# Performance work log

Hardware: AMD Instinct MI355X
Metric: run time of the kernel (lower is better)

The kernel has to match this reference:

```python
import jax, jax.numpy as jnp
import numpy as np

B, C_IN, C_OUT, T, HID = 8, 32, 32, 8192, 64


def setup_inputs() -> dict:
    key = jax.random.key(0)
    ks = jax.random.split(key, 8)
    s1 = 1.0  # fan_in=1
    s2 = 1.0 / np.sqrt(HID)
    return {
        "x": jax.random.normal(ks[0], (B, C_IN, T), dtype=jnp.float32),
        "w1": jax.random.uniform(ks[1], (1, HID), jnp.float32, -s1, s1),
        "b1": jax.random.uniform(ks[2], (HID,), jnp.float32, -s1, s1),
        "w2": jax.random.uniform(ks[3], (HID, HID), jnp.float32, -s2, s2),
        "b2": jax.random.uniform(ks[4], (HID,), jnp.float32, -s2, s2),
        "w3": jax.random.uniform(ks[5], (HID, C_IN * C_OUT), jnp.float32, -s2, s2),
        "b3": jax.random.uniform(ks[6], (C_IN * C_OUT,), jnp.float32, -s2, s2),
        "bias": jnp.zeros((C_OUT,), dtype=jnp.float32),
    }


def _filters(w1, b1, w2, b2, w3, b3):
    # positions: (T, 1) in [0, 1]
    pos = jnp.linspace(0.0, 1.0, T, dtype=jnp.float32)[:, None]
    h = jax.nn.gelu(pos @ w1 + b1, approximate=False)
    h = jax.nn.gelu(h @ w2 + b2, approximate=False)
    f = h @ w3 + b3                      # (T, out*in)
    f = f.reshape(T, C_OUT, C_IN)
    return jnp.transpose(f, (1, 2, 0))   # (out, in, T)


def reference(x, w1, b1, w2, b2, w3, b3, bias):
    freq_x = jnp.fft.rfft(x, axis=-1)                      # (B, in, F)
    filt = _filters(w1, b1, w2, b2, w3, b3)                # (out, in, T)
    freq_f = jnp.fft.rfft(filt, axis=-1)                   # (out, in, F)
    conv_freq = jnp.einsum('bif,oif->bof', freq_x, freq_f) # contract over in
    out = jnp.fft.irfft(conv_freq, n=T, axis=-1)           # (B, out, T)
    return out + bias[None, :, None]
```

## Files before the change

kernel.cpp:

```cpp
#include <hip/hip_runtime.h>
#include <math.h>

#define T 8192
#define M 4096
#define JS 4104
#define B 8
#define CIN 32
#define COUT 32
#define HID 64
#define FT 4

__device__ inline float2 cadd(float2 a, float2 b){ return make_float2(a.x+b.x, a.y+b.y); }
__device__ inline float2 csub(float2 a, float2 b){ return make_float2(a.x-b.x, a.y-b.y); }
__device__ inline float2 cmul(float2 a, float2 b){ return make_float2(a.x*b.x - a.y*b.y, a.x*b.y + a.y*b.x); }
__device__ inline float2 cmulc(float2 a, float2 b){
    return make_float2(a.x*b.x + a.y*b.y, a.y*b.x - a.x*b.y); }
__device__ inline int swz(int p){ return p ^ ((p >> 5) & 31); }
__device__ inline int brev12(int v){ return (int)(__brev((unsigned)v) >> 20); }

__device__ inline float gelu_exact(float x){
    return 0.5f*x*(1.0f + erff(x*0.70710678118654752440f));
}

__global__ __launch_bounds__(256) void tw_init(float2* __restrict__ tw){
    int k = blockIdx.x*blockDim.x + threadIdx.x;
    float ang = -6.28318530717958647692f * (float)k / (float)T;
    float s, c;
    sincosf(ang, &s, &c);
    tw[k] = make_float2(c, s);
}

template<int S, int SH0>
__device__ inline void dif_group8(float2 q[8], int r, const float2* __restrict__ tw){
    #pragma unroll
    for (int st = 0; st < 3; ++st){
        const int d = 4 >> st;
        const int sh = SH0 + st;
        #pragma unroll
        for (int k = 0; k < 4; ++k){
            const int jd = k & (d-1);
            const int lo = ((k & ~(d-1)) << 1) | jd;
            const int hi = lo + d;
            float2 w = tw[(r + S*jd) << sh];
            float2 a = q[lo], b = q[hi];
            q[lo] = cadd(a, b);
            q[hi] = cmul(csub(a, b), w);
        }
    }
}
template<int S, int SH0>
__device__ inline void dit_group8(float2 q[8], int r, const float2* __restrict__ tw){
    #pragma unroll
    for (int st = 0; st < 3; ++st){
        const int d = 1 << st;
        const int sh = SH0 - st;
        #pragma unroll
        for (int k = 0; k < 4; ++k){
            const int jd = k & (d-1);
            const int lo = ((k & ~(d-1)) << 1) | jd;
            const int hi = lo + d;
            float2 w = tw[(r + S*jd) << sh];
            float2 a = q[lo];
            float2 t2 = cmulc(q[hi], w);
            q[lo] = cadd(a, t2);
            q[hi] = csub(a, t2);
        }
    }
}

__device__ inline void lds_store8(float* sRe, float* sIm, const float2* q, int base, int S){
    #pragma unroll
    for (int l = 0; l < 8; ++l){ int a = swz(base + S*l); sRe[a] = q[l].x; sIm[a] = q[l].y; }
}
__device__ inline void lds_load8(const float* sRe, const float* sIm, float2* q, int base, int S){
    #pragma unroll
    for (int l = 0; l < 8; ++l){ int a = swz(base + S*l); q[l] = make_float2(sRe[a], sIm[a]); }
}

__global__ __launch_bounds__(512) void rfft_fwd(const float* __restrict__ src,
        const float2* __restrict__ tw, float2* __restrict__ dst){
    __shared__ float sRe[M], sIm[M];
    const int t = threadIdx.x;
    const int sig = blockIdx.x;
    const float2* zp = (const float2*)(src + (size_t)sig*T);
    float2 q[8];
    #pragma unroll
    for (int l = 0; l < 8; ++l) q[l] = zp[t + 512*l];
    dif_group8<512,1>(q, t, tw);
    lds_store8(sRe, sIm, q, t, 512);
    __syncthreads();
    {
        const int base = ((t>>6)<<9) | (t&63);
        lds_load8(sRe, sIm, q, base, 64);
        dif_group8<64,4>(q, t&63, tw);
        lds_store8(sRe, sIm, q, base, 64);
    }
    __syncthreads();
    {
        const int base = ((t>>3)<<6) | (t&7);
        lds_load8(sRe, sIm, q, base, 8);
        dif_group8<8,7>(q, t&7, tw);
        lds_store8(sRe, sIm, q, base, 8);
    }
    __syncthreads();
    {
        const int base = t << 3;
        lds_load8(sRe, sIm, q, base, 1);
        dif_group8<1,10>(q, 0, tw);
        lds_store8(sRe, sIm, q, base, 1);
    }
    __syncthreads();
    float2* dp = dst + (size_t)sig*JS;
    #pragma unroll
    for (int l = 0; l < 8; ++l){
        const int j  = t + 512*l;
        const int k  = brev12(j);
        const int j2 = brev12((M - k) & (M-1));
        float2 Z  = make_float2(sRe[swz(j)],  sIm[swz(j)]);
        float2 Zm = make_float2(sRe[swz(j2)], sIm[swz(j2)]);
        float2 E = make_float2(0.5f*(Z.x + Zm.x), 0.5f*(Z.y - Zm.y));
        float2 D = make_float2(Z.x - Zm.x, Z.y + Zm.y);
        float2 O = make_float2(0.5f*D.y, -0.5f*D.x);
        dp[j] = cadd(E, cmul(tw[k], O));
        if (j == 0) dp[M] = make_float2(Z.x - Z.y, 0.0f);
    }
}

__global__ __launch_bounds__(512) void irfft_out(const float2* __restrict__ Yh,
        const float2* __restrict__ tw, const float* __restrict__ bias, float* __restrict__ out){
    __shared__ float sRe[M], sIm[M];
    const int t = threadIdx.x;
    const int sig = blockIdx.x;
    const float2* yp = Yh + (size_t)sig*JS;
    #pragma unroll
    for (int l = 0; l < 8; ++l){
        const int j = t + 512*l;
        float2 v = yp[j];
        sRe[swz(j)] = v.x; sIm[swz(j)] = v.y;
    }
    float2 yM = yp[M];
    __syncthreads();
    #pragma unroll
    for (int l = 0; l < 8; ++l){
        const int j = t + 512*l;
        const int k = brev12(j);
        if (k <= 2048){
            float2 Ym; int j2 = 0;
            if (k == 0){ Ym = yM; }
            else { j2 = brev12((M - k) & (M-1)); Ym = make_float2(sRe[swz(j2)], sIm[swz(j2)]); }
            float2 Y = make_float2(sRe[swz(j)], sIm[swz(j)]);
            float2 E = make_float2(0.5f*(Y.x + Ym.x), 0.5f*(Y.y - Ym.y));
            float2 D = make_float2(0.5f*(Y.x - Ym.x), 0.5f*(Y.y + Ym.y));
            float2 O = cmulc(D, tw[k]);
            sRe[swz(j)] = E.x - O.y;  sIm[swz(j)] = E.y + O.x;
            if (k != 0 && k != 2048){
                sRe[swz(j2)] = E.x + O.y;  sIm[swz(j2)] = O.x - E.y;
            }
        }
    }
    __syncthreads();
    float2 q[8];
    {
        const int base = t << 3;
        lds_load8(sRe, sIm, q, base, 1);
        dit_group8<1,12>(q, 0, tw);
        lds_store8(sRe, sIm, q, base, 1);
    }
    __syncthreads();
    {
        const int base = ((t>>3)<<6) | (t&7);
        lds_load8(sRe, sIm, q, base, 8);
        dit_group8<8,9>(q, t&7, tw);
        lds_store8(sRe, sIm, q, base, 8);
    }
    __syncthreads();
    {
        const int base = ((t>>6)<<9) | (t&63);
        lds_load8(sRe, sIm, q, base, 64);
        dit_group8<64,6>(q, t&63, tw);
        lds_store8(sRe, sIm, q, base, 64);
    }
    __syncthreads();
    lds_load8(sRe, sIm, q, t, 512);
    dit_group8<512,3>(q, t, tw);
    const float sc = 1.0f/(float)M;
    const float bv = bias[sig & (COUT-1)];
    float2* op = (float2*)(out + (size_t)sig*T);
    #pragma unroll
    for (int l = 0; l < 8; ++l)
        op[t + 512*l] = make_float2(q[l].x*sc + bv, q[l].y*sc + bv);
}

#define TB 32
__global__ __launch_bounds__(256) void mlp_hidden(const float* __restrict__ w1, const float* __restrict__ b1,
                           const float* __restrict__ w2, const float* __restrict__ b2,
                           float* __restrict__ H){
    __shared__ float sw1[HID], sb1[HID], sw2[HID*HID], sb2[HID];
    __shared__ float h1s[TB][HID+1];
    const int tid = threadIdx.x;
    for (int i = tid; i < HID; i += 256){ sw1[i]=w1[i]; sb1[i]=b1[i]; sb2[i]=b2[i]; }
    for (int i = tid; i < HID*HID; i += 256) sw2[i]=w2[i];
    __syncthreads();
    const int t0 = blockIdx.x * TB;
    for (int e = tid; e < TB*HID; e += 256){
        const int tl = e & (TB-1), h = e >> 5;
        const float pos = (float)(t0 + tl) / (float)(T-1);
        h1s[tl][h] = gelu_exact(pos*sw1[h] + sb1[h]);
    }
    __syncthreads();
    const int tl = tid & (TB-1), hg = tid >> 5;
    float acc[8];
    #pragma unroll
    for (int u = 0; u < 8; ++u) acc[u] = sb2[hg*8 + u];
    for (int k = 0; k < HID; ++k){
        const float hv = h1s[tl][k];
        const float4 wa = *(const float4*)&sw2[k*HID + hg*8];
        const float4 wb = *(const float4*)&sw2[k*HID + hg*8 + 4];
        acc[0] += hv*wa.x; acc[1] += hv*wa.y; acc[2] += hv*wa.z; acc[3] += hv*wa.w;
        acc[4] += hv*wb.x; acc[5] += hv*wb.y; acc[6] += hv*wb.z; acc[7] += hv*wb.w;
    }
    #pragma unroll
    for (int u = 0; u < 8; ++u)
        H[(size_t)(hg*8 + u)*T + t0 + tl] = gelu_exact(acc[u]);
}

__global__ __launch_bounds__(256) void filt_contract(const float* __restrict__ w3,
        const float* __restrict__ b3, const float2* __restrict__ Hh,
        const float2* __restrict__ Xh, float2* __restrict__ Yh){
    __shared__ float2 Xs[B][CIN][FT];
    __shared__ float2 FiltS[512][FT];
    const int t = threadIdx.x;
    const int f0 = blockIdx.x * FT;
    const int oh = blockIdx.y;
    {
        const float2* xp = Xh + (size_t)t*JS + f0;
        float2 v0 = xp[0], v1 = xp[1], v2 = xp[2], v3 = xp[3];
        const int b = t >> 5, i = t & 31;
        Xs[b][i][0] = v0; Xs[b][i][1] = v1; Xs[b][i][2] = v2; Xs[b][i][3] = v3;
    }
    const int oiL = t << 1;
    const int oiG = oh*512 + oiL;
    float2 acc[2][FT];
    #pragma unroll
    for (int ii = 0; ii < 2; ++ii)
        #pragma unroll
        for (int f = 0; f < FT; ++f) acc[ii][f] = make_float2(0.f, 0.f);
    for (int h = 0; h < HID; ++h){
        const float2 w2v = *(const float2*)(w3 + (size_t)h*(CIN*COUT) + oiG);
        const float2* hp = Hh + (size_t)h*JS + f0;
        float2 h0 = hp[0], h1 = hp[1], h2 = hp[2], h3 = hp[3];
        const float wv[2] = {w2v.x, w2v.y};
        #pragma unroll
        for (int ii = 0; ii < 2; ++ii){
            acc[ii][0].x += wv[ii]*h0.x; acc[ii][0].y += wv[ii]*h0.y;
            acc[ii][1].x += wv[ii]*h1.x; acc[ii][1].y += wv[ii]*h1.y;
            acc[ii][2].x += wv[ii]*h2.x; acc[ii][2].y += wv[ii]*h2.y;
            acc[ii][3].x += wv[ii]*h3.x; acc[ii][3].y += wv[ii]*h3.y;
        }
    }
    if (f0 == 0){
        #pragma unroll
        for (int ii = 0; ii < 2; ++ii)
            acc[ii][0].x += (float)T * b3[oiG + ii];
    }
    #pragma unroll
    for (int ii = 0; ii < 2; ++ii)
        #pragma unroll
        for (int f = 0; f < FT; ++f)
            FiltS[oiL + ii][f] = acc[ii][f];
    __syncthreads();
    const int o2 = t >> 4, f2 = (t >> 2) & 3, g = t & 3;
    float2 y[2];
    y[0] = make_float2(0.f, 0.f); y[1] = make_float2(0.f, 0.f);
    #pragma unroll 4
    for (int i0 = 0; i0 < CIN; ++i0){
        const int i = (i0 + o2) & 31;
        const float2 fv = FiltS[(o2 << 5) | i][f2];
        #pragma unroll
        for (int j = 0; j < 2; ++j){
            const float2 xv = Xs[(g << 1) | j][i][f2];
            y[j].x += xv.x*fv.x - xv.y*fv.y;
            y[j].y += xv.x*fv.y + xv.y*fv.x;
        }
    }
    if (f0 + f2 <= M){
        #pragma unroll
        for (int j = 0; j < 2; ++j){
            const int b = (g << 1) | j;
            const int o = oh*16 + o2;
            Yh[((size_t)(b*COUT + o))*JS + f0 + f2] = y[j];
        }
    }
}

extern "C" void kernel_launch(void* const* d_in, const int* in_sizes, int n_in,
                              void* d_out, int out_size, void* d_ws, size_t ws_size,
                              hipStream_t stream){
    const float* x    = (const float*)d_in[0];
    const float* w1   = (const float*)d_in[1];
    const float* b1   = (const float*)d_in[2];
    const float* w2   = (const float*)d_in[3];
    const float* b2   = (const float*)d_in[4];
    const float* w3   = (const float*)d_in[5];
    const float* b3   = (const float*)d_in[6];
    const float* bias = (const float*)d_in[7];
    float* out = (float*)d_out;

    char* ws = (char*)d_ws;
    float2* Xh = (float2*)ws;
    float2* Yh = (float2*)(ws + (size_t)9*1024*1024);
    float2* Hh = (float2*)(ws + (size_t)18*1024*1024);
    float*  H  = (float*) (ws + (size_t)21*1024*1024);
    float2* tws= (float2*)(ws + (size_t)23*1024*1024);

    hipLaunchKernelGGL(tw_init,       dim3(16),    dim3(256), 0, stream, tws);
    hipLaunchKernelGGL(mlp_hidden,    dim3(T/TB),  dim3(256), 0, stream, w1, b1, w2, b2, H);
    hipLaunchKernelGGL(rfft_fwd,      dim3(B*CIN), dim3(512), 0, stream, x, tws, Xh);
    hipLaunchKernelGGL(rfft_fwd,      dim3(HID),   dim3(512), 0, stream, H, tws, Hh);
    hipLaunchKernelGGL(filt_contract, dim3(M/FT + 1, 2), dim3(256), 0, stream, w3, b3, Hh, Xh, Yh);
    hipLaunchKernelGGL(irfft_out,     dim3(B*COUT), dim3(512), 0, stream, Yh, tws, bias, out);
}
```

Before: 159.0 us.

## Merge forward FFT launches, interleave LDS complex storage, relayout contraction shared memory

```diff
diff --git a/kernel.cpp b/kernel.cpp
--- a/kernel.cpp
+++ b/kernel.cpp
@@ -68,56 +68,60 @@
     }
 }
 
-__device__ inline void lds_store8(float* sRe, float* sIm, const float2* q, int base, int S){
-    #pragma unroll
-    for (int l = 0; l < 8; ++l){ int a = swz(base + S*l); sRe[a] = q[l].x; sIm[a] = q[l].y; }
-}
-__device__ inline void lds_load8(const float* sRe, const float* sIm, float2* q, int base, int S){
-    #pragma unroll
-    for (int l = 0; l < 8; ++l){ int a = swz(base + S*l); q[l] = make_float2(sRe[a], sIm[a]); }
-}
-
-__global__ __launch_bounds__(512) void rfft_fwd(const float* __restrict__ src,
-        const float2* __restrict__ tw, float2* __restrict__ dst){
-    __shared__ float sRe[M], sIm[M];
+__device__ inline void lds_store8(float2* sc, const float2* q, int base, int S){
+    #pragma unroll
+    for (int l = 0; l < 8; ++l) sc[swz(base + S*l)] = q[l];
+}
+__device__ inline void lds_load8(const float2* sc, float2* q, int base, int S){
+    #pragma unroll
+    for (int l = 0; l < 8; ++l) q[l] = sc[swz(base + S*l)];
+}
+
+__global__ __launch_bounds__(512) void rfft_all(const float* __restrict__ x,
+        const float* __restrict__ H, const float2* __restrict__ tw,
+        float2* __restrict__ Xh, float2* __restrict__ Hh){
+    __shared__ float2 sc[M];
     const int t = threadIdx.x;
     const int sig = blockIdx.x;
-    const float2* zp = (const float2*)(src + (size_t)sig*T);
+    const float* srow;
+    float2* dp;
+    if (sig < B*CIN){ srow = x + (size_t)sig*T;        dp = Xh + (size_t)sig*JS; }
+    else            { srow = H + (size_t)(sig-B*CIN)*T; dp = Hh + (size_t)(sig-B*CIN)*JS; }
+    const float2* zp = (const float2*)srow;
     float2 q[8];
     #pragma unroll
     for (int l = 0; l < 8; ++l) q[l] = zp[t + 512*l];
     dif_group8<512,1>(q, t, tw);
-    lds_store8(sRe, sIm, q, t, 512);
+    lds_store8(sc, q, t, 512);
     __syncthreads();
     {
         const int base = ((t>>6)<<9) | (t&63);
-        lds_load8(sRe, sIm, q, base, 64);
+        lds_load8(sc, q, base, 64);
         dif_group8<64,4>(q, t&63, tw);
-        lds_store8(sRe, sIm, q, base, 64);
+        lds_store8(sc, q, base, 64);
     }
     __syncthreads();
     {
         const int base = ((t>>3)<<6) | (t&7);
-        lds_load8(sRe, sIm, q, base, 8);
+        lds_load8(sc, q, base, 8);
         dif_group8<8,7>(q, t&7, tw);
-        lds_store8(sRe, sIm, q, base, 8);
+        lds_store8(sc, q, base, 8);
     }
     __syncthreads();
     {
         const int base = t << 3;
-        lds_load8(sRe, sIm, q, base, 1);
+        lds_load8(sc, q, base, 1);
         dif_group8<1,10>(q, 0, tw);
-        lds_store8(sRe, sIm, q, base, 1);
-    }
-    __syncthreads();
-    float2* dp = dst + (size_t)sig*JS;
+        lds_store8(sc, q, base, 1);
+    }
+    __syncthreads();
     #pragma unroll
     for (int l = 0; l < 8; ++l){
         const int j  = t + 512*l;
         const int k  = brev12(j);
         const int j2 = brev12((M - k) & (M-1));
-        float2 Z  = make_float2(sRe[swz(j)],  sIm[swz(j)]);
-        float2 Zm = make_float2(sRe[swz(j2)], sIm[swz(j2)]);
+        float2 Z  = sc[swz(j)];
+        float2 Zm = sc[swz(j2)];
         float2 E = make_float2(0.5f*(Z.x + Zm.x), 0.5f*(Z.y - Zm.y));
         float2 D = make_float2(Z.x - Zm.x, Z.y + Zm.y);
         float2 O = make_float2(0.5f*D.y, -0.5f*D.x);
@@ -128,15 +132,14 @@
 
 __global__ __launch_bounds__(512) void irfft_out(const float2* __restrict__ Yh,
         const float2* __restrict__ tw, const float* __restrict__ bias, float* __restrict__ out){
-    __shared__ float sRe[M], sIm[M];
+    __shared__ float2 sc[M];
     const int t = threadIdx.x;
     const int sig = blockIdx.x;
     const float2* yp = Yh + (size_t)sig*JS;
     #pragma unroll
     for (int l = 0; l < 8; ++l){
         const int j = t + 512*l;
-        float2 v = yp[j];
-        sRe[swz(j)] = v.x; sIm[swz(j)] = v.y;
+        sc[swz(j)] = yp[j];
     }
     float2 yM = yp[M];
     __syncthreads();
@@ -147,14 +150,14 @@
         if (k <= 2048){
             float2 Ym; int j2 = 0;
             if (k == 0){ Ym = yM; }
-            else { j2 = brev12((M - k) & (M-1)); Ym = make_float2(sRe[swz(j2)], sIm[swz(j2)]); }
-            float2 Y = make_float2(sRe[swz(j)], sIm[swz(j)]);
+            else { j2 = brev12((M - k) & (M-1)); Ym = sc[swz(j2)]; }
+            float2 Y = sc[swz(j)];
             float2 E = make_float2(0.5f*(Y.x + Ym.x), 0.5f*(Y.y - Ym.y));
             float2 D = make_float2(0.5f*(Y.x - Ym.x), 0.5f*(Y.y + Ym.y));
             float2 O = cmulc(D, tw[k]);
-            sRe[swz(j)] = E.x - O.y;  sIm[swz(j)] = E.y + O.x;
+            sc[swz(j)] = make_float2(E.x - O.y, E.y + O.x);
             if (k != 0 && k != 2048){
-                sRe[swz(j2)] = E.x + O.y;  sIm[swz(j2)] = O.x - E.y;
+                sc[swz(j2)] = make_float2(E.x + O.y, O.x - E.y);
             }
         }
     }
@@ -162,33 +165,33 @@
     float2 q[8];
     {
         const int base = t << 3;
-        lds_load8(sRe, sIm, q, base, 1);
+        lds_load8(sc, q, base, 1);
         dit_group8<1,12>(q, 0, tw);
-        lds_store8(sRe, sIm, q, base, 1);
+        lds_store8(sc, q, base, 1);
     }
     __syncthreads();
     {
         const int base = ((t>>3)<<6) | (t&7);
-        lds_load8(sRe, sIm, q, base, 8);
+        lds_load8(sc, q, base, 8);
         dit_group8<8,9>(q, t&7, tw);
-        lds_store8(sRe, sIm, q, base, 8);
+        lds_store8(sc, q, base, 8);
     }
     __syncthreads();
     {
         const int base = ((t>>6)<<9) | (t&63);
-        lds_load8(sRe, sIm, q, base, 64);
+        lds_load8(sc, q, base, 64);
         dit_group8<64,6>(q, t&63, tw);
-        lds_store8(sRe, sIm, q, base, 64);
-    }
-    __syncthreads();
-    lds_load8(sRe, sIm, q, t, 512);
+        lds_store8(sc, q, base, 64);
+    }
+    __syncthreads();
+    lds_load8(sc, q, t, 512);
     dit_group8<512,3>(q, t, tw);
-    const float sc = 1.0f/(float)M;
+    const float scv = 1.0f/(float)M;
     const float bv = bias[sig & (COUT-1)];
     float2* op = (float2*)(out + (size_t)sig*T);
     #pragma unroll
     for (int l = 0; l < 8; ++l)
-        op[t + 512*l] = make_float2(q[l].x*sc + bv, q[l].y*sc + bv);
+        op[t + 512*l] = make_float2(q[l].x*scv + bv, q[l].y*scv + bv);
 }
 
 #define TB 32
@@ -227,24 +230,29 @@
 __global__ __launch_bounds__(256) void filt_contract(const float* __restrict__ w3,
         const float* __restrict__ b3, const float2* __restrict__ Hh,
         const float2* __restrict__ Xh, float2* __restrict__ Yh){
-    __shared__ float2 Xs[B][CIN][FT];
-    __shared__ float2 FiltS[512][FT];
+    __shared__ float XsRe[CIN][FT][B+1];
+    __shared__ float XsIm[CIN][FT][B+1];
+    __shared__ float FltRe[FT][16][33];
+    __shared__ float FltIm[FT][16][33];
     const int t = threadIdx.x;
     const int f0 = blockIdx.x * FT;
     const int oh = blockIdx.y;
     {
-        const float2* xp = Xh + (size_t)t*JS + f0;
-        float2 v0 = xp[0], v1 = xp[1], v2 = xp[2], v3 = xp[3];
+        const float4* xp4 = (const float4*)(Xh + (size_t)t*JS + f0);
+        float4 u0 = xp4[0], u1 = xp4[1];
         const int b = t >> 5, i = t & 31;
-        Xs[b][i][0] = v0; Xs[b][i][1] = v1; Xs[b][i][2] = v2; Xs[b][i][3] = v3;
-    }
-    const int oiL = t << 1;
-    const int oiG = oh*512 + oiL;
+        XsRe[i][0][b] = u0.x; XsIm[i][0][b] = u0.y;
+        XsRe[i][1][b] = u0.z; XsIm[i][1][b] = u0.w;
+        XsRe[i][2][b] = u1.x; XsIm[i][2][b] = u1.y;
+        XsRe[i][3][b] = u1.z; XsIm[i][3][b] = u1.w;
+    }
+    const int oiG = oh*512 + (t << 1);
     float2 acc[2][FT];
     #pragma unroll
     for (int ii = 0; ii < 2; ++ii)
         #pragma unroll
         for (int f = 0; f < FT; ++f) acc[ii][f] = make_float2(0.f, 0.f);
+    #pragma unroll 4
     for (int h = 0; h < HID; ++h){
         const float2 w2v = *(const float2*)(w3 + (size_t)h*(CIN*COUT) + oiG);
         const float2* hp = Hh + (size_t)h*JS + f0;
@@ -263,22 +271,28 @@
         for (int ii = 0; ii < 2; ++ii)
             acc[ii][0].x += (float)T * b3[oiG + ii];
     }
-    #pragma unroll
-    for (int ii = 0; ii < 2; ++ii)
-        #pragma unroll
-        for (int f = 0; f < FT; ++f)
-            FiltS[oiL + ii][f] = acc[ii][f];
+    {
+        const int oL = t >> 4;
+        const int ib = (t & 15) << 1;
+        #pragma unroll
+        for (int ii = 0; ii < 2; ++ii)
+            #pragma unroll
+            for (int f = 0; f < FT; ++f){
+                FltRe[f][oL][ib + ii] = acc[ii][f].x;
+                FltIm[f][oL][ib + ii] = acc[ii][f].y;
+            }
+    }
     __syncthreads();
     const int o2 = t >> 4, f2 = (t >> 2) & 3, g = t & 3;
     float2 y[2];
     y[0] = make_float2(0.f, 0.f); y[1] = make_float2(0.f, 0.f);
-    #pragma unroll 4
+    #pragma unroll 8
     for (int i0 = 0; i0 < CIN; ++i0){
-        const int i = (i0 + o2) & 31;
-        const float2 fv = FiltS[(o2 << 5) | i][f2];
+        const float2 fv = make_float2(FltRe[f2][o2][i0], FltIm[f2][o2][i0]);
         #pragma unroll
         for (int j = 0; j < 2; ++j){
-            const float2 xv = Xs[(g << 1) | j][i][f2];
+            const int b = (g << 1) | j;
+            const float2 xv = make_float2(XsRe[i0][f2][b], XsIm[i0][f2][b]);
             y[j].x += xv.x*fv.x - xv.y*fv.y;
             y[j].y += xv.x*fv.y + xv.y*fv.x;
         }
@@ -313,10 +327,9 @@
     float*  H  = (float*) (ws + (size_t)21*1024*1024);
     float2* tws= (float2*)(ws + (size_t)23*1024*1024);
 
-    hipLaunchKernelGGL(tw_init,       dim3(16),    dim3(256), 0, stream, tws);
-    hipLaunchKernelGGL(mlp_hidden,    dim3(T/TB),  dim3(256), 0, stream, w1, b1, w2, b2, H);
-    hipLaunchKernelGGL(rfft_fwd,      dim3(B*CIN), dim3(512), 0, stream, x, tws, Xh);
-    hipLaunchKernelGGL(rfft_fwd,      dim3(HID),   dim3(512), 0, stream, H, tws, Hh);
+    hipLaunchKernelGGL(tw_init,       dim3(16),        dim3(256), 0, stream, tws);
+    hipLaunchKernelGGL(mlp_hidden,    dim3(T/TB),      dim3(256), 0, stream, w1, b1, w2, b2, H);
+    hipLaunchKernelGGL(rfft_all,      dim3(B*CIN+HID), dim3(512), 0, stream, x, H, tws, Xh, Hh);
     hipLaunchKernelGGL(filt_contract, dim3(M/FT + 1, 2), dim3(256), 0, stream, w3, b3, Hh, Xh, Yh);
-    hipLaunchKernelGGL(irfft_out,     dim3(B*COUT), dim3(512), 0, stream, Yh, tws, bias, out);
-}
+    hipLaunchKernelGGL(irfft_out,     dim3(B*COUT),    dim3(512), 0, stream, Yh, tws, bias, out);
+}
```

New measurement: 147.8 us. 7.0% less time.
